# Kernel optimization log

Hardware: AMD Instinct MI355X
Metric: run time of the kernel (lower is better)

The kernel has to match this reference:

```python
import jax, jax.numpy as jnp
import numpy as np

IN_DIM = 512
OUT_DIM = 512
NUM_HARMONICS = 32
BATCH = 4096


def setup_inputs() -> dict:
    key = jax.random.key(0)
    k1, k2 = jax.random.split(key)
    x = jax.random.normal(k1, (BATCH, IN_DIM), dtype=jnp.float32)
    std = 1.0 / np.sqrt(IN_DIM * NUM_HARMONICS)
    fourier_coeffs = jax.random.normal(
        k2, (IN_DIM, NUM_HARMONICS, 2, OUT_DIM), dtype=jnp.float32) * std
    bias = jnp.zeros((OUT_DIM,), dtype=jnp.float32)
    return {"x": x, "fourier_coeffs": fourier_coeffs, "bias": bias}


def reference(x, fourier_coeffs, bias):
    # k = [1, ..., num_harmonics]
    k = jnp.arange(1, fourier_coeffs.shape[1] + 1, dtype=x.dtype)
    kx = x[:, :, None] * k                      # [b, i, g]
    trig = jnp.stack([jnp.cos(kx), jnp.sin(kx)], axis=-1)  # [b, i, g, 2]
    out = jnp.einsum('bigf,igfo->bo', trig, fourier_coeffs)
    return out + bias
```

## Files before the change

kernel.cpp:

```cpp
#include <hip/hip_runtime.h>
#include <hip/hip_bf16.h>
#include <stdint.h>
#include <stddef.h>

#define BATCH   4096
#define INDIM   512
#define OUTDIM  512
#define NH      32
#define KKDIM   64
#define INV2PI  0.15915494309189535f

#define BM       128
#define BN       128
#define THREADS  256
#define KSPLIT   8
#define DIMS_PER_WG (INDIM / KSPLIT)
#define CHUNK_COLS  256
#define CHUNK_ELEMS (CHUNK_COLS * KKDIM)

#define B_BYTES       16384
#define SMEM_BYTES    (2 * B_BYTES)

typedef short  bhalf8  __attribute__((ext_vector_type(8)));
typedef float  vfloat4 __attribute__((ext_vector_type(4)));

union AFrag { uint4 u; bhalf8 h; };

__device__ __forceinline__ unsigned pack_bf16(float a, float b) {
    union { __hip_bfloat162 h2; unsigned u; } cv;
    cv.h2 = __float22bfloat162_rn(float2{a, b});
    return cv.u;
}

__device__ __forceinline__ void async_copy16(const void* gsrc, void* ldst) {
    __builtin_amdgcn_global_load_lds(
        (const __attribute__((address_space(1))) void*)(uintptr_t)gsrc,
        (__attribute__((address_space(3))) void*)(uint32_t)(uintptr_t)ldst,
        16, 0, 0);
}

__global__ __launch_bounds__(256) void fkan_prepass(const float* __restrict__ coeffs,
                                                    unsigned short* __restrict__ Bt) {
    __shared__ float lds[64][260];
    const int t  = threadIdx.x;
    const int cb = blockIdx.x & 1;
    const int i  = blockIdx.x >> 1;
    const float* __restrict__ src = coeffs + (size_t)i * (KKDIM * OUTDIM) + cb * CHUNK_COLS;
    unsigned short* __restrict__ chunk = Bt + (size_t)(cb * INDIM + i) * CHUNK_ELEMS;
#pragma unroll
    for (int rd = 0; rd < 16; ++rd) {
        const int r  = rd * 4 + (t >> 6);
        const int c4 = (t & 63) * 4;
        const float4 v = *(const float4*)(src + (size_t)r * OUTDIM + c4);
        *(float4*)&lds[r][c4] = v;
    }
    __syncthreads();
#pragma unroll
    for (int s = 0; s < 8; ++s) {
        const int unit = t + s * 256;
        const int col  = unit >> 3;
        const int pc   = unit & 7;
        const int kb   = (pc ^ (col & 7)) * 8;
        uint4 o;
        o.x = pack_bf16(lds[kb + 0][col], lds[kb + 1][col]);
        o.y = pack_bf16(lds[kb + 2][col], lds[kb + 3][col]);
        o.z = pack_bf16(lds[kb + 4][col], lds[kb + 5][col]);
        o.w = pack_bf16(lds[kb + 6][col], lds[kb + 7][col]);
        ((uint4*)chunk)[unit] = o;
    }
}

__global__ __launch_bounds__(256) void fkan_bias_init(const float* __restrict__ bias,
                                                      float* __restrict__ out) {
    const int idx = blockIdx.x * 256 + threadIdx.x;
    ((float4*)out)[idx] = ((const float4*)bias)[idx & 127];
}

__device__ __forceinline__ void stage_B(const char* __restrict__ chunk_half, char* smem,
                                        int parity, int t) {
    char* bdst = smem + parity * B_BYTES;
#pragma unroll
    for (int s = 0; s < 4; ++s) {
        const int unit = t + s * 256;
        async_copy16(chunk_half + unit * 16, bdst + unit * 16);
    }
}

__device__ __forceinline__ void make_av(float rv, float k0f, float k1f,
                                        bhalf8* a0, bhalf8* a1) {
    const float cd = __builtin_amdgcn_cosf(rv);
    const float sd = __builtin_amdgcn_sinf(rv);
    AFrag A;
    float c = __builtin_amdgcn_cosf(k0f * rv);
    float s = __builtin_amdgcn_sinf(k0f * rv);
    A.u.x = pack_bf16(c, s);
    { const float nc = c*cd - s*sd, ns = s*cd + c*sd; c = nc; s = ns; }
    A.u.y = pack_bf16(c, s);
    { const float nc = c*cd - s*sd, ns = s*cd + c*sd; c = nc; s = ns; }
    A.u.z = pack_bf16(c, s);
    { const float nc = c*cd - s*sd, ns = s*cd + c*sd; c = nc; s = ns; }
    A.u.w = pack_bf16(c, s);
    *a0 = A.h;
    c = __builtin_amdgcn_cosf(k1f * rv);
    s = __builtin_amdgcn_sinf(k1f * rv);
    A.u.x = pack_bf16(c, s);
    { const float nc = c*cd - s*sd, ns = s*cd + c*sd; c = nc; s = ns; }
    A.u.y = pack_bf16(c, s);
    { const float nc = c*cd - s*sd, ns = s*cd + c*sd; c = nc; s = ns; }
    A.u.z = pack_bf16(c, s);
    { const float nc = c*cd - s*sd, ns = s*cd + c*sd; c = nc; s = ns; }
    A.u.w = pack_bf16(c, s);
    *a1 = A.h;
}

#define MFMA_BLOCK(Bb, A0, A1)                                                  \
    do {                                                                        \
        _Pragma("unroll")                                                       \
        for (int ct = 0; ct < 8; ++ct) {                                        \
            const int cbyte = (ct * 16 + fr) * 128;                             \
            const bhalf8 b0 = *(const bhalf8*)((Bb) + cbyte + off0);            \
            acc[0][ct] = __builtin_amdgcn_mfma_f32_16x16x32_bf16(               \
                (A0)[0], b0, acc[0][ct], 0, 0, 0);                              \
            acc[1][ct] = __builtin_amdgcn_mfma_f32_16x16x32_bf16(               \
                (A0)[1], b0, acc[1][ct], 0, 0, 0);                              \
            const bhalf8 b1 = *(const bhalf8*)((Bb) + cbyte + off1);            \
            acc[0][ct] = __builtin_amdgcn_mfma_f32_16x16x32_bf16(               \
                (A1)[0], b1, acc[0][ct], 0, 0, 0);                              \
            acc[1][ct] = __builtin_amdgcn_mfma_f32_16x16x32_bf16(               \
                (A1)[1], b1, acc[1][ct], 0, 0, 0);                              \
        }                                                                       \
    } while (0)

__global__ __launch_bounds__(THREADS, 3) void fkan_main(const float* __restrict__ x,
                                                        const unsigned short* __restrict__ Bt,
                                                        float* __restrict__ out) {
    __shared__ char smem[SMEM_BYTES];
    const int t      = threadIdx.x;
    const int grp    = blockIdx.x & 31;
    const int member = blockIdx.x >> 5;
    const int kq      = grp & 7;
    const int cb4     = grp >> 3;
    const int cb2     = cb4 >> 1;
    const int rowbase = member * BM;
    const int colbase = cb4 * BN;
    const int dimbase = kq * DIMS_PER_WG;

    const int lane = t & 63;
    const int w    = t >> 6;
    const int fr   = lane & 15;
    const int fq   = lane >> 4;
    const int fx   = lane & 7;
    const int off0 = (fq ^ fx) * 16;
    const int off1 = ((4 + fq) ^ fx) * 16;

    const float k0f = (float)(fq * 4 + 1);
    const float k1f = (float)(fq * 4 + 17);

    const float* __restrict__ xp0 = x + (size_t)(rowbase + w * 32 + fr) * INDIM + dimbase;
    const float* __restrict__ xp1 = xp0 + (size_t)16 * INDIM;

    const char* __restrict__ chunkbase =
        (const char*)(Bt + (size_t)(cb2 * INDIM + dimbase) * CHUNK_ELEMS) + (cb4 & 1) * 16384;

    vfloat4 acc[2][8];
#pragma unroll
    for (int a = 0; a < 2; ++a)
#pragma unroll
        for (int b = 0; b < 8; ++b) acc[a][b] = (vfloat4)0.0f;

    bhalf8 a0A[2], a1A[2], a0B[2], a1B[2];
    stage_B(chunkbase, smem, 0, t);
    make_av(xp0[0] * INV2PI, k0f, k1f, &a0A[0], &a1A[0]);
    make_av(xp1[0] * INV2PI, k0f, k1f, &a0A[1], &a1A[1]);
    __syncthreads();

    for (int it2 = 0; it2 < DIMS_PER_WG; it2 += 2) {
        {
            const int inxt = it2 + 1;
            stage_B(chunkbase + (size_t)inxt * 32768, smem, 1, t);
            make_av(xp0[inxt] * INV2PI, k0f, k1f, &a0B[0], &a1B[0]);
            make_av(xp1[inxt] * INV2PI, k0f, k1f, &a0B[1], &a1B[1]);
            MFMA_BLOCK(smem, a0A, a1A);
            __syncthreads();
        }
        {
            const int inxt = it2 + 2;
            if (inxt < DIMS_PER_WG) {
                stage_B(chunkbase + (size_t)inxt * 32768, smem, 0, t);
                make_av(xp0[inxt] * INV2PI, k0f, k1f, &a0A[0], &a1A[0]);
                make_av(xp1[inxt] * INV2PI, k0f, k1f, &a0A[1], &a1A[1]);
            }
            MFMA_BLOCK(smem + B_BYTES, a0B, a1B);
            __syncthreads();
        }
    }

#pragma unroll
    for (int rt = 0; rt < 2; ++rt) {
#pragma unroll
        for (int ct = 0; ct < 8; ++ct) {
            const int col  = colbase + ct * 16 + fr;
            const int row0 = rowbase + w * 32 + rt * 16 + fq * 4;
#pragma unroll
            for (int r = 0; r < 4; ++r)
                atomicAdd(out + (size_t)(row0 + r) * OUTDIM + col, acc[rt][ct][r]);
        }
    }
}

__global__ __launch_bounds__(256) void fkan_naive(const float* __restrict__ x,
                                                  const float* __restrict__ coeffs,
                                                  const float* __restrict__ bias,
                                                  float* __restrict__ out) {
    const int b = blockIdx.x >> 1;
    const int o = ((blockIdx.x & 1) << 8) + threadIdx.x;
    float acc = bias[o];
    const float* xrow = x + (size_t)b * INDIM;
    for (int i = 0; i < INDIM; ++i) {
        const float rv = xrow[i] * INV2PI;
        const float cd = __builtin_amdgcn_cosf(rv);
        const float sd = __builtin_amdgcn_sinf(rv);
        float c = cd, s = sd;
        const float* cp = coeffs + (size_t)i * (KKDIM * OUTDIM) + o;
#pragma unroll 4
        for (int g = 0; g < NH; ++g) {
            acc += c * cp[g * 2 * OUTDIM] + s * cp[(g * 2 + 1) * OUTDIM];
            const float nc = c * cd - s * sd;
            const float ns = s * cd + c * sd;
            c = nc; s = ns;
        }
    }
    out[(size_t)b * OUTDIM + o] = acc;
}

extern "C" void kernel_launch(void* const* d_in, const int* in_sizes, int n_in,
                              void* d_out, int out_size, void* d_ws, size_t ws_size,
                              hipStream_t stream) {
    (void)in_sizes; (void)n_in; (void)out_size;
    const float* x      = (const float*)d_in[0];
    const float* coeffs = (const float*)d_in[1];
    const float* bias   = (const float*)d_in[2];
    float* out          = (float*)d_out;

    const size_t bt_bytes = (size_t)2 * INDIM * CHUNK_ELEMS * sizeof(unsigned short);
    if (ws_size >= bt_bytes) {
        unsigned short* Bt = (unsigned short*)d_ws;
        fkan_prepass<<<2 * INDIM, 256, 0, stream>>>(coeffs, Bt);
        fkan_bias_init<<<(BATCH * OUTDIM) / (4 * 256), 256, 0, stream>>>(bias, out);
        fkan_main<<<(BATCH / BM) * (OUTDIM / BN) * KSPLIT, THREADS, 0, stream>>>(x, Bt, out);
    } else {
        fkan_naive<<<BATCH * 2, 256, 0, stream>>>(x, coeffs, bias, out);
    }
}
```

Measured before the change: 287.2 us.

## Use partial vmcnt waits with split barriers and compute A-fragments just in time

Replaces __syncthreads with inline s_waitcnt vmcnt(4) + s_barrier, so the next stage's global loads (presumably direct-to-LDS) can stay in flight while the current buffer is consumed. A post-MFMA barrier protects buffer reuse. A-operand trig fragments are now computed per iteration instead of being double-buffered in registers, and launch_bounds occupancy goes from 3 to 5 to raise waves per SIMD. This relies on stage_B issuing exactly the assumed number of vm ops. It also risks register spills under the tighter bound.

```diff
diff --git a/kernel.cpp b/kernel.cpp
--- a/kernel.cpp
+++ b/kernel.cpp
@@ -131,7 +131,11 @@
         }                                                                       \
     } while (0)
 
-__global__ __launch_bounds__(THREADS, 3) void fkan_main(const float* __restrict__ x,
+#define WAITBAR4 asm volatile("s_waitcnt vmcnt(4)\n\ts_barrier" ::: "memory")
+#define WAITBAR0 asm volatile("s_waitcnt vmcnt(0)\n\ts_barrier" ::: "memory")
+#define POSTBAR  asm volatile("s_barrier" ::: "memory")
+
+__global__ __launch_bounds__(THREADS, 5) void fkan_main(const float* __restrict__ x,
                                                         const unsigned short* __restrict__ Bt,
                                                         float* __restrict__ out) {
     __shared__ char smem[SMEM_BYTES];
@@ -168,31 +172,26 @@
 #pragma unroll
         for (int b = 0; b < 8; ++b) acc[a][b] = (vfloat4)0.0f;
 
-    bhalf8 a0A[2], a1A[2], a0B[2], a1B[2];
     stage_B(chunkbase, smem, 0, t);
-    make_av(xp0[0] * INV2PI, k0f, k1f, &a0A[0], &a1A[0]);
-    make_av(xp1[0] * INV2PI, k0f, k1f, &a0A[1], &a1A[1]);
-    __syncthreads();
-
-    for (int it2 = 0; it2 < DIMS_PER_WG; it2 += 2) {
-        {
-            const int inxt = it2 + 1;
-            stage_B(chunkbase + (size_t)inxt * 32768, smem, 1, t);
-            make_av(xp0[inxt] * INV2PI, k0f, k1f, &a0B[0], &a1B[0]);
-            make_av(xp1[inxt] * INV2PI, k0f, k1f, &a0B[1], &a1B[1]);
-            MFMA_BLOCK(smem, a0A, a1A);
-            __syncthreads();
-        }
-        {
-            const int inxt = it2 + 2;
-            if (inxt < DIMS_PER_WG) {
-                stage_B(chunkbase + (size_t)inxt * 32768, smem, 0, t);
-                make_av(xp0[inxt] * INV2PI, k0f, k1f, &a0A[0], &a1A[0]);
-                make_av(xp1[inxt] * INV2PI, k0f, k1f, &a0A[1], &a1A[1]);
-            }
-            MFMA_BLOCK(smem + B_BYTES, a0B, a1B);
-            __syncthreads();
-        }
+
+#pragma unroll 2
+    for (int it = 0; it < DIMS_PER_WG - 1; ++it) {
+        const int p = it & 1;
+        stage_B(chunkbase + (size_t)(it + 1) * 32768, smem, p ^ 1, t);
+        bhalf8 a0[2], a1[2];
+        make_av(xp0[it] * INV2PI, k0f, k1f, &a0[0], &a1[0]);
+        make_av(xp1[it] * INV2PI, k0f, k1f, &a0[1], &a1[1]);
+        WAITBAR4;
+        MFMA_BLOCK(smem + p * B_BYTES, a0, a1);
+        POSTBAR;
+    }
+    {
+        const int it = DIMS_PER_WG - 1;
+        bhalf8 a0[2], a1[2];
+        make_av(xp0[it] * INV2PI, k0f, k1f, &a0[0], &a1[0]);
+        make_av(xp1[it] * INV2PI, k0f, k1f, &a0[1], &a1[1]);
+        WAITBAR0;
+        MFMA_BLOCK(smem + (it & 1) * B_BYTES, a0, a1);
     }
 
 #pragma unroll
```

Result: slower. 327.1 us (+13.9%).

## Stage two input dims per barrier and fuse bias init into prepass

Applied to the files above, without the earlier changes.

The main loop now double-buffers pairs of input dimensions (32 KB per stage), halving the number of block barriers, and loads x as float2 pairs. Trig A-fragments are computed just before their MFMAs instead of being prefetched, and s_setprio raises wave priority around the MFMA blocks. The bias-init kernel is folded into the prepass to save a launch. LDS use doubles to 64 KB and launch bounds drop to 2 blocks per CU, trading occupancy for fewer syncs.

```diff
diff --git a/kernel.cpp b/kernel.cpp
--- a/kernel.cpp
+++ b/kernel.cpp
@@ -18,8 +18,8 @@
 #define CHUNK_COLS  256
 #define CHUNK_ELEMS (CHUNK_COLS * KKDIM)
 
-#define B_BYTES       16384
-#define SMEM_BYTES    (2 * B_BYTES)
+#define PAIR_BYTES    32768
+#define SMEM_BYTES    (2 * PAIR_BYTES)
 
 typedef short  bhalf8  __attribute__((ext_vector_type(8)));
 typedef float  vfloat4 __attribute__((ext_vector_type(4)));
@@ -40,9 +40,17 @@
 }
 
 __global__ __launch_bounds__(256) void fkan_prepass(const float* __restrict__ coeffs,
-                                                    unsigned short* __restrict__ Bt) {
+                                                    unsigned short* __restrict__ Bt,
+                                                    const float* __restrict__ bias,
+                                                    float* __restrict__ out) {
     __shared__ float lds[64][260];
     const int t  = threadIdx.x;
+    {
+        const int gidx = blockIdx.x * 256 + t;
+        const float4 bv = ((const float4*)bias)[gidx & 127];
+        ((float4*)out)[gidx] = bv;
+        ((float4*)out)[gidx + 262144] = bv;
+    }
     const int cb = blockIdx.x & 1;
     const int i  = blockIdx.x >> 1;
     const float* __restrict__ src = coeffs + (size_t)i * (KKDIM * OUTDIM) + cb * CHUNK_COLS;
@@ -70,19 +78,17 @@
     }
 }
 
-__global__ __launch_bounds__(256) void fkan_bias_init(const float* __restrict__ bias,
-                                                      float* __restrict__ out) {
-    const int idx = blockIdx.x * 256 + threadIdx.x;
-    ((float4*)out)[idx] = ((const float4*)bias)[idx & 127];
-}
-
-__device__ __forceinline__ void stage_B(const char* __restrict__ chunk_half, char* smem,
-                                        int parity, int t) {
-    char* bdst = smem + parity * B_BYTES;
-#pragma unroll
-    for (int s = 0; s < 4; ++s) {
-        const int unit = t + s * 256;
-        async_copy16(chunk_half + unit * 16, bdst + unit * 16);
+__device__ __forceinline__ void stage_pair(const char* __restrict__ chunkbase, int d0,
+                                           char* smem, int buf, int t) {
+#pragma unroll
+    for (int dd = 0; dd < 2; ++dd) {
+        const char* gsrc = chunkbase + (size_t)(d0 + dd) * 32768;
+        char* ldst = smem + buf * PAIR_BYTES + dd * 16384;
+#pragma unroll
+        for (int s = 0; s < 4; ++s) {
+            const int unit = t + s * 256;
+            async_copy16(gsrc + unit * 16, ldst + unit * 16);
+        }
     }
 }
 
@@ -131,7 +137,7 @@
         }                                                                       \
     } while (0)
 
-__global__ __launch_bounds__(THREADS, 3) void fkan_main(const float* __restrict__ x,
+__global__ __launch_bounds__(THREADS, 2) void fkan_main(const float* __restrict__ x,
                                                         const unsigned short* __restrict__ Bt,
                                                         float* __restrict__ out) {
     __shared__ char smem[SMEM_BYTES];
@@ -156,8 +162,10 @@
     const float k0f = (float)(fq * 4 + 1);
     const float k1f = (float)(fq * 4 + 17);
 
-    const float* __restrict__ xp0 = x + (size_t)(rowbase + w * 32 + fr) * INDIM + dimbase;
-    const float* __restrict__ xp1 = xp0 + (size_t)16 * INDIM;
+    const float2* __restrict__ xr0 =
+        (const float2*)(x + (size_t)(rowbase + w * 32 + fr) * INDIM + dimbase);
+    const float2* __restrict__ xr1 =
+        (const float2*)(x + (size_t)(rowbase + w * 32 + 16 + fr) * INDIM + dimbase);
 
     const char* __restrict__ chunkbase =
         (const char*)(Bt + (size_t)(cb2 * INDIM + dimbase) * CHUNK_ELEMS) + (cb4 & 1) * 16384;
@@ -168,31 +176,39 @@
 #pragma unroll
         for (int b = 0; b < 8; ++b) acc[a][b] = (vfloat4)0.0f;
 
-    bhalf8 a0A[2], a1A[2], a0B[2], a1B[2];
-    stage_B(chunkbase, smem, 0, t);
-    make_av(xp0[0] * INV2PI, k0f, k1f, &a0A[0], &a1A[0]);
-    make_av(xp1[0] * INV2PI, k0f, k1f, &a0A[1], &a1A[1]);
+    float2 cq0 = xr0[0], cq1 = xr1[0];
+    float2 nq0, nq1;
+    stage_pair(chunkbase, 0, smem, 0, t);
     __syncthreads();
 
-    for (int it2 = 0; it2 < DIMS_PER_WG; it2 += 2) {
+#pragma unroll 1
+    for (int g = 0; g < 32; ++g) {
+        const int p = g & 1;
+        if (g < 31) {
+            stage_pair(chunkbase, 2 * g + 2, smem, p ^ 1, t);
+            nq0 = xr0[g + 1];
+            nq1 = xr1[g + 1];
+        }
         {
-            const int inxt = it2 + 1;
-            stage_B(chunkbase + (size_t)inxt * 32768, smem, 1, t);
-            make_av(xp0[inxt] * INV2PI, k0f, k1f, &a0B[0], &a1B[0]);
-            make_av(xp1[inxt] * INV2PI, k0f, k1f, &a0B[1], &a1B[1]);
-            MFMA_BLOCK(smem, a0A, a1A);
-            __syncthreads();
+            bhalf8 a0[2], a1[2];
+            make_av(cq0.x * INV2PI, k0f, k1f, &a0[0], &a1[0]);
+            make_av(cq1.x * INV2PI, k0f, k1f, &a0[1], &a1[1]);
+            const char* Bb = smem + p * PAIR_BYTES;
+            __builtin_amdgcn_s_setprio(1);
+            MFMA_BLOCK(Bb, a0, a1);
+            __builtin_amdgcn_s_setprio(0);
         }
         {
-            const int inxt = it2 + 2;
-            if (inxt < DIMS_PER_WG) {
-                stage_B(chunkbase + (size_t)inxt * 32768, smem, 0, t);
-                make_av(xp0[inxt] * INV2PI, k0f, k1f, &a0A[0], &a1A[0]);
-                make_av(xp1[inxt] * INV2PI, k0f, k1f, &a0A[1], &a1A[1]);
-            }
-            MFMA_BLOCK(smem + B_BYTES, a0B, a1B);
-            __syncthreads();
-        }
+            bhalf8 a0[2], a1[2];
+            make_av(cq0.y * INV2PI, k0f, k1f, &a0[0], &a1[0]);
+            make_av(cq1.y * INV2PI, k0f, k1f, &a0[1], &a1[1]);
+            const char* Bb = smem + p * PAIR_BYTES + 16384;
+            __builtin_amdgcn_s_setprio(1);
+            MFMA_BLOCK(Bb, a0, a1);
+            __builtin_amdgcn_s_setprio(0);
+        }
+        cq0 = nq0; cq1 = nq1;
+        __syncthreads();
     }
 
 #pragma unroll
@@ -245,8 +261,7 @@
     const size_t bt_bytes = (size_t)2 * INDIM * CHUNK_ELEMS * sizeof(unsigned short);
     if (ws_size >= bt_bytes) {
         unsigned short* Bt = (unsigned short*)d_ws;
-        fkan_prepass<<<2 * INDIM, 256, 0, stream>>>(coeffs, Bt);
-        fkan_bias_init<<<(BATCH * OUTDIM) / (4 * 256), 256, 0, stream>>>(bias, out);
+        fkan_prepass<<<2 * INDIM, 256, 0, stream>>>(coeffs, Bt, bias, out);
         fkan_main<<<(BATCH / BM) * (OUTDIM / BN) * KSPLIT, THREADS, 0, stream>>>(x, Bt, out);
     } else {
         fkan_naive<<<BATCH * 2, 256, 0, stream>>>(x, coeffs, bias, out);
```

Result: no change. 282.7 us (-1.6%).
